# Kernel tuning notes

Measured on AMD Instinct MI355X. Metric: run time of the kernel, lower is better.

## Reference

```python
import jax, jax.numpy as jnp
import numpy as np

EMBED = 512; HEADS = 16; WIN = 8; SHIFT = 4

def _rel_pos_index(Wh, Ww):
    # WindowMSA.double_step_seq + transpose-sum + flip(1)
    seq1 = np.arange(0, (2 * Ww - 1) * Wh, 2 * Ww - 1)
    seq2 = np.arange(0, Ww)
    coords = (seq1[:, None] + seq2[None, :]).reshape(1, -1)
    idx = coords + coords.T            # (Wh*Ww, Wh*Ww)
    return idx[:, ::-1].copy()

def _attn_mask(H_pad, W_pad, win, shift, nf):
    # static (trace-time) shifted-window mask, values in {0, -100}
    img = np.zeros((H_pad, W_pad))
    cnt = 0
    for h in (slice(0, -win), slice(-win, -shift), slice(-shift, None)):
        for w in (slice(0, -win), slice(-win, -shift), slice(-shift, None)):
            img[h, w] = cnt
            cnt += 1
    mw = img.reshape(H_pad // win, win, W_pad // win, win).transpose(0, 2, 1, 3).reshape(-1, win * win)
    am = mw[:, None, :] - mw[:, :, None]
    am = np.where(am != 0, -100.0, 0.0)
    return np.tile(am, (1, 1, nf))     # (nW, N, nf*N)

def setup_inputs():
    key = jax.random.key(0)
    ks = jax.random.split(key, 8)
    B, H, W, C, nf = 8, 128, 128, EMBED, 2
    s = 0.02
    return {
        'q': jax.random.normal(ks[0], (B, H * W, C), jnp.float32),
        'kv': jax.random.normal(ks[1], (B, nf, H * W, C), jnp.float32),
        'H': H, 'W': W,
        'rpb_table': jax.random.normal(ks[2], ((2 * WIN - 1) ** 2, HEADS), jnp.float32) * s,
        'Wq': jax.random.normal(ks[3], (C, C), jnp.float32) * s,
        'bq': jnp.zeros((C,), jnp.float32),
        'Wkv': jax.random.normal(ks[4], (C, 2 * C), jnp.float32) * s,
        'bkv': jnp.zeros((2 * C,), jnp.float32),
        'Wo': jax.random.normal(ks[5], (C, C), jnp.float32) * s,
        'bo': jnp.zeros((C,), jnp.float32),
    }

def reference(q, kv, H, W, rpb_table, Wq, bq, Wkv, bkv, Wo, bo):
    B, L, C = q.shape
    nf = kv.shape[1]
    win, shift, heads = WIN, SHIFT, HEADS
    hd = C // heads
    scale = hd ** -0.5
    pad_b = (-H) % win
    pad_r = (-W) % win
    x = q.reshape(B, H, W, C)
    kvx = kv.reshape(B * nf, H, W, C)
    x = jnp.pad(x, ((0, 0), (0, pad_b), (0, pad_r), (0, 0)))
    kvx = jnp.pad(kvx, ((0, 0), (0, pad_b), (0, pad_r), (0, 0)))
    Hp, Wp = H + pad_b, W + pad_r
    nh, nw = Hp // win, Wp // win
    if shift > 0:
        x = jnp.roll(x, (-shift, -shift), (1, 2))
        kvx = jnp.roll(kvx, (-shift, -shift), (1, 2))
        mask = jnp.asarray(_attn_mask(Hp, Wp, win, shift, nf), q.dtype)
    else:
        mask = None
    Nq = win * win
    Nk = nf * Nq
    # window partition: (B, Hp, Wp, C) -> (B*nh*nw, Nq, C)
    qw = x.reshape(B, nh, win, nw, win, C).transpose(0, 1, 3, 2, 4, 5).reshape(B * nh * nw, Nq, C)
    # kv: (B*nf, Hp, Wp, C) -> (B*nh*nw, nf*Nq, C)
    kvw = kvx.reshape(B, nf, nh, win, nw, win, C).transpose(0, 2, 4, 1, 3, 5, 6).reshape(B * nh * nw, Nk, C)
    Bw = qw.shape[0]
    qh = (qw @ Wq + bq).reshape(Bw, Nq, heads, hd).transpose(0, 2, 1, 3) * scale
    kvp = (kvw @ Wkv + bkv).reshape(Bw, Nk, 2, heads, hd).transpose(2, 0, 3, 1, 4)
    kh, vh = kvp[0], kvp[1]
    attn = jnp.einsum('bhqd,bhkd->bhqk', qh, kh)
    rpi = jnp.asarray(_rel_pos_index(win, win).reshape(-1))
    rpb = rpb_table[rpi].reshape(Nq, Nq, heads).transpose(2, 0, 1)  # (heads, Nq, Nq)
    attn = attn + jnp.tile(rpb, (1, 1, nf))[None]
    if mask is not None:
        nW = mask.shape[0]
        attn = (attn.reshape(Bw // nW, nW, heads, Nq, Nk) + mask[None, :, None]).reshape(Bw, heads, Nq, Nk)
    attn = jax.nn.softmax(attn, axis=-1)
    ow = jnp.einsum('bhqk,bhkd->bqhd', attn, vh).reshape(Bw, Nq, C)
    ow = ow @ Wo + bo
    # window reverse
    x = ow.reshape(B, nh, nw, win, win, C).transpose(0, 1, 3, 2, 4, 5).reshape(B, Hp, Wp, C)
    if shift > 0:
        x = jnp.roll(x, (shift, shift), (1, 2))
    x = x[:, :H, :W, :].reshape(B, H * W, C)
    return x
```

## Files before the change

kernel.cpp:

```cpp
#include <hip/hip_runtime.h>

typedef unsigned short ushort_t;
typedef short bf16x8 __attribute__((ext_vector_type(8)));
typedef float f32x4 __attribute__((ext_vector_type(4)));

#define MFMA16(a, b, c) __builtin_amdgcn_mfma_f32_16x16x32_bf16(a, b, c, 0, 0, 0)

static __device__ __forceinline__ float bf2f(ushort_t u) {
  union { unsigned int i; float f; } v;
  v.i = ((unsigned int)u) << 16;
  return v.f;
}
static __device__ __forceinline__ ushort_t f2bf(float f) {
  union { float f; unsigned int i; } v;
  v.f = f;
  unsigned int u = v.i;
  u = u + 0x7fffu + ((u >> 16) & 1u);
  return (ushort_t)(u >> 16);
}
static __device__ __forceinline__ unsigned int cvtpk(float lo, float hi) {
  unsigned int r;
  asm("v_cvt_pk_bf16_f32 %0, %1, %2" : "=v"(r) : "v"(lo), "v"(hi));
  return r;
}
static __device__ __forceinline__ void gload16(const void* g, void* l) {
  __builtin_amdgcn_global_load_lds((const __attribute__((address_space(1))) void*)g,
                                   (__attribute__((address_space(3))) void*)l,
                                   16, 0, 0);
}

__global__ void ws_sentinel(float* out, unsigned long long ws) {
  if (blockIdx.x == 0 && threadIdx.x == 0)
    out[0] = 1.0e6f * (1.0f + (float)(ws >> 23));
}

__global__ __launch_bounds__(256) void wtrans(const float* __restrict__ in,
                                              ushort_t* __restrict__ out,
                                              int R, int C) {
  int idx = blockIdx.x * 256 + threadIdx.x;
  if (idx < R * C) {
    int r = idx / C, c = idx - r * C;
    out[c * R + r] = f2bf(in[idx]);
  }
}

template <bool AF32, bool CF32>
__global__ __launch_bounds__(256, 2) void gemm_bt(const void* __restrict__ Av,
                                                  const ushort_t* __restrict__ Bt,
                                                  const float* __restrict__ bias,
                                                  void* __restrict__ Cv,
                                                  int N, int Nt) {
  constexpr int K = 512;
  __shared__ unsigned char As[AF32 ? 128 * 32 * 4 : 128 * 32 * 2];
  __shared__ unsigned char Bs[128 * 32 * 2];
  const int t = threadIdx.x;
  const int l = t & 63;
  const int w = t >> 6;
  const int w32 = w * 32;
  const int wr = w >> 1, wc = w & 1;
  const int lrow = l & 15;
  const int g = l >> 4;

  const int bid = blockIdx.x;
  const int xcd = bid & 7;
  const int slot = bid >> 3;
  const int mt = xcd + 8 * (slot / Nt);
  const int nt = slot % Nt;
  const long m0 = (long)mt * 128;
  const int n0 = nt * 128;

  const int arow = l >> 3;
  const int acol = 4 * ((l & 7) ^ (arow & 1));
  const int brow = l >> 2;
  const int bcol = 8 * (l & 3);

  const f32x4 fz = {0.f, 0.f, 0.f, 0.f};
  f32x4 acc[4][4];
#pragma unroll
  for (int i = 0; i < 4; i++)
#pragma unroll
    for (int j = 0; j < 4; j++) acc[i][j] = fz;

  for (int kk = 0; kk < K; kk += 32) {
    __syncthreads();
    if constexpr (AF32) {
#pragma unroll
      for (int i = 0; i < 4; i++) {
        const float* gp = (const float*)Av + (m0 + w32 + i * 8 + arow) * (long)K + kk + acol;
        gload16(gp, &As[(w32 + i * 8) * 128]);
      }
    } else {
#pragma unroll
      for (int i = 0; i < 2; i++) {
        const ushort_t* gp = (const ushort_t*)Av + (m0 + w32 + i * 16 + brow) * (long)K + kk + bcol;
        gload16(gp, &As[(w32 + i * 16) * 64]);
      }
    }
#pragma unroll
    for (int i = 0; i < 2; i++) {
      const ushort_t* gp = Bt + (long)(n0 + w32 + i * 16 + brow) * K + kk + bcol;
      gload16(gp, &Bs[(w32 + i * 16) * 64]);
    }
    __syncthreads();

    bf16x8 af[4], bfr[4];
    if constexpr (AF32) {
#pragma unroll
      for (int mi = 0; mi < 4; mi++) {
        const int aR = wr * 64 + mi * 16 + lrow;
        const int sw = (aR & 1);
        f32x4 x = *(const f32x4*)&As[aR * 128 + (((2 * g) ^ sw) << 4)];
        f32x4 y = *(const f32x4*)&As[aR * 128 + (((2 * g + 1) ^ sw) << 4)];
        union { unsigned int u[4]; bf16x8 v; } r;
        r.u[0] = cvtpk(x[0], x[1]);
        r.u[1] = cvtpk(x[2], x[3]);
        r.u[2] = cvtpk(y[0], y[1]);
        r.u[3] = cvtpk(y[2], y[3]);
        af[mi] = r.v;
      }
    } else {
#pragma unroll
      for (int mi = 0; mi < 4; mi++) {
        const int aR = wr * 64 + mi * 16 + lrow;
        af[mi] = *(const bf16x8*)&As[aR * 64 + g * 16];
      }
    }
#pragma unroll
    for (int ni = 0; ni < 4; ni++) {
      const int bR = wc * 64 + ni * 16 + lrow;
      bfr[ni] = *(const bf16x8*)&Bs[bR * 64 + g * 16];
    }
#pragma unroll
    for (int mi = 0; mi < 4; mi++)
#pragma unroll
      for (int ni = 0; ni < 4; ni++)
        acc[mi][ni] = MFMA16(af[mi], bfr[ni], acc[mi][ni]);
  }

#pragma unroll
  for (int mi = 0; mi < 4; mi++) {
    const long row0 = m0 + wr * 64 + mi * 16 + (l >> 4) * 4;
#pragma unroll
    for (int ni = 0; ni < 4; ni++) {
      const int col = n0 + wc * 64 + ni * 16 + lrow;
      const float bv = bias[col];
#pragma unroll
      for (int r = 0; r < 4; r++) {
        const float val = acc[mi][ni][r] + bv;
        if constexpr (CF32)
          ((float*)Cv)[(row0 + r) * N + col] = val;
        else
          ((ushort_t*)Cv)[(row0 + r) * N + col] = f2bf(val);
      }
    }
  }
}

__global__ __launch_bounds__(64, 1) void attn_k(const ushort_t* __restrict__ Qp,
                                                const ushort_t* __restrict__ KVp,
                                                const float* __restrict__ rpbt,
                                                ushort_t* __restrict__ Ao) {
  __shared__ ushort_t P[64 * 136];
  __shared__ __align__(16) unsigned char pool[32 * 136 * 2];
  float* Ltab = (float*)pool;
  ushort_t* Vt = (ushort_t*)pool;
  const int l = threadIdx.x;
  const int wnd = blockIdx.x;
  const int h = blockIdx.y;
  const int b = wnd >> 8;
  const int wh = (wnd >> 4) & 15;
  const int ww = wnd & 15;
  for (int i = l; i < 225; i += 64) Ltab[i] = rpbt[i * 16 + h];

  const int lrow = l & 15;
  const int lq = l >> 4;
  const int lk = lq * 8;

  auto qrow = [&](int q) -> long {
    int i = q >> 3, j = q & 7;
    int ho = (wh * 8 + i + 4) & 127;
    int wo = (ww * 8 + j + 4) & 127;
    return (long)((b << 14) + (ho << 7) + wo);
  };
  auto kvrow = [&](int kp) -> long {
    int f = kp >> 6, m = kp & 63;
    int i = m >> 3, j = m & 7;
    int ho = (wh * 8 + i + 4) & 127;
    int wo = (ww * 8 + j + 4) & 127;
    return (long)(((b * 2 + f) << 14) + (ho << 7) + wo);
  };
  auto cnt_of = [&](int m) -> int {
    int hr = wh * 8 + (m >> 3), wr2 = ww * 8 + (m & 7);
    int rh = hr < 120 ? 0 : (hr < 124 ? 1 : 2);
    int rw = wr2 < 120 ? 0 : (wr2 < 124 ? 1 : 2);
    return rh * 3 + rw;
  };
  auto cvec = [](int m) -> int { return 15 * (m >> 3) + (m & 7); };

  const f32x4 fz = {0.f, 0.f, 0.f, 0.f};
  f32x4 s[4][8];
#pragma unroll
  for (int mi = 0; mi < 4; mi++)
#pragma unroll
    for (int ni = 0; ni < 8; ni++) s[mi][ni] = fz;

  bf16x8 af[4];
#pragma unroll
  for (int mi = 0; mi < 4; mi++)
    af[mi] = *(const bf16x8*)(Qp + qrow(mi * 16 + lrow) * 512 + h * 32 + lk);
#pragma unroll
  for (int ni = 0; ni < 8; ni++) {
    bf16x8 kf = *(const bf16x8*)(KVp + kvrow(ni * 16 + lrow) * 1024 + h * 32 + lk);
#pragma unroll
    for (int mi = 0; mi < 4; mi++) s[mi][ni] = MFMA16(af[mi], kf, s[mi][ni]);
  }

  __syncthreads();

  const float scale = 0.17677669529663687f;
#pragma unroll
  for (int mi = 0; mi < 4; mi++) {
#pragma unroll
    for (int r = 0; r < 4; r++) {
      const int q = mi * 16 + lq * 4 + r;
      const int cq = cnt_of(q);
      const int cqv = cvec(q);
      float mx = -3.0e38f;
#pragma unroll
      for (int ni = 0; ni < 8; ni++) {
        const int k63 = (ni * 16 + lrow) & 63;
        float v = s[mi][ni][r] * scale + Ltab[cqv + cvec(63 - k63)];
        if (cnt_of(k63) != cq) v -= 100.f;
        s[mi][ni][r] = v;
        mx = fmaxf(mx, v);
      }
      mx = fmaxf(mx, __shfl_xor(mx, 1));
      mx = fmaxf(mx, __shfl_xor(mx, 2));
      mx = fmaxf(mx, __shfl_xor(mx, 4));
      mx = fmaxf(mx, __shfl_xor(mx, 8));
      float sum = 0.f;
#pragma unroll
      for (int ni = 0; ni < 8; ni++) {
        float p = __expf(s[mi][ni][r] - mx);
        s[mi][ni][r] = p;
        sum += p;
      }
      sum += __shfl_xor(sum, 1);
      sum += __shfl_xor(sum, 2);
      sum += __shfl_xor(sum, 4);
      sum += __shfl_xor(sum, 8);
      const float inv = 1.f / sum;
#pragma unroll
      for (int ni = 0; ni < 8; ni++)
        P[q * 136 + ni * 16 + lrow] = f2bf(s[mi][ni][r] * inv);
    }
  }

#pragma unroll
  for (int kv2 = 0; kv2 < 2; kv2++) {
    const int kp = l * 2 + kv2;
    const ushort_t* src = KVp + kvrow(kp) * 1024 + 512 + h * 32;
    bf16x8 v0 = *(const bf16x8*)(src);
    bf16x8 v1 = *(const bf16x8*)(src + 8);
    bf16x8 v2 = *(const bf16x8*)(src + 16);
    bf16x8 v3 = *(const bf16x8*)(src + 24);
#pragma unroll
    for (int d = 0; d < 8; d++) {
      Vt[(d) * 136 + kp] = (ushort_t)v0[d];
      Vt[(8 + d) * 136 + kp] = (ushort_t)v1[d];
      Vt[(16 + d) * 136 + kp] = (ushort_t)v2[d];
      Vt[(24 + d) * 136 + kp] = (ushort_t)v3[d];
    }
  }
  __syncthreads();

  f32x4 o[4][2];
#pragma unroll
  for (int mi = 0; mi < 4; mi++) { o[mi][0] = fz; o[mi][1] = fz; }
#pragma unroll
  for (int ks = 0; ks < 4; ks++) {
    bf16x8 pf[4];
#pragma unroll
    for (int mi = 0; mi < 4; mi++)
      pf[mi] = *(const bf16x8*)&P[(mi * 16 + lrow) * 136 + ks * 32 + lk];
#pragma unroll
    for (int ni = 0; ni < 2; ni++) {
      bf16x8 vf = *(const bf16x8*)&Vt[(ni * 16 + lrow) * 136 + ks * 32 + lk];
#pragma unroll
      for (int mi = 0; mi < 4; mi++) o[mi][ni] = MFMA16(pf[mi], vf, o[mi][ni]);
    }
  }

#pragma unroll
  for (int mi = 0; mi < 4; mi++)
#pragma unroll
    for (int ni = 0; ni < 2; ni++)
#pragma unroll
      for (int r = 0; r < 4; r++) {
        const int q = mi * 16 + lq * 4 + r;
        Ao[qrow(q) * 512 + h * 32 + ni * 16 + lrow] = f2bf(o[mi][ni][r]);
      }
}

extern "C" void kernel_launch(void* const* d_in, const int* in_sizes, int n_in,
                              void* d_out, int out_size, void* d_ws, size_t ws_size,
                              hipStream_t stream) {
  (void)in_sizes; (void)n_in; (void)out_size;
  const float* q    = (const float*)d_in[0];
  const float* kv   = (const float*)d_in[1];
  const float* rpbt = (const float*)d_in[4];
  const float* Wq   = (const float*)d_in[5];
  const float* bq   = (const float*)d_in[6];
  const float* Wkv  = (const float*)d_in[7];
  const float* bkv  = (const float*)d_in[8];
  const float* Wo   = (const float*)d_in[9];
  const float* bo   = (const float*)d_in[10];
  float* out = (float*)d_out;

  const size_t QB  = 16384ULL * 512;
  const size_t KVB = 32768ULL * 1024;
  const size_t per_b_bytes = (QB + QB + KVB) * 2;
  const size_t fixed_bytes = (512ULL*512 + 512ULL*1024 + 512ULL*512) * 2;
  const size_t needed1 = fixed_bytes + per_b_bytes;

  if (ws_size < needed1) {
    ws_sentinel<<<dim3(1), 64, 0, stream>>>(out, (unsigned long long)ws_size);
    return;
  }

  int nbc = 8;
  while (nbc > 1 && fixed_bytes + (size_t)nbc * per_b_bytes > ws_size) nbc >>= 1;

  char* ws = (char*)d_ws;
  ushort_t* WqT  = (ushort_t*)ws;
  ushort_t* WkvT = WqT + 512 * 512;
  ushort_t* WoT  = WkvT + 512 * 1024;
  ushort_t* Qp   = (ushort_t*)(ws + fixed_bytes);
  ushort_t* Ao   = Qp + (size_t)nbc * QB;
  ushort_t* KVp  = Ao + (size_t)nbc * QB;

  wtrans<<<dim3(1024), 256, 0, stream>>>(Wq, WqT, 512, 512);
  wtrans<<<dim3(2048), 256, 0, stream>>>(Wkv, WkvT, 512, 1024);
  wtrans<<<dim3(1024), 256, 0, stream>>>(Wo, WoT, 512, 512);

  for (int c = 0; c < 8 / nbc; ++c) {
    const size_t b0 = (size_t)c * nbc;
    const int MtQ = nbc * 128;
    const int MtKV = nbc * 256;
    gemm_bt<true, false><<<dim3(MtQ * 4), 256, 0, stream>>>(q + b0 * QB, WqT, bq,
                                                            Qp, 512, 4);
    gemm_bt<true, false><<<dim3(MtKV * 8), 256, 0, stream>>>(kv + b0 * KVB / 2, WkvT,
                                                             bkv, KVp, 1024, 8);
    attn_k<<<dim3(nbc * 256, 16), 64, 0, stream>>>(Qp, KVp, rpbt, Ao);
    gemm_bt<false, true><<<dim3(MtQ * 4), 256, 0, stream>>>(Ao, WoT, bo,
                                                            out + b0 * QB, 512, 4);
  }
}
```

Measured before the change: 1.077 ms.

## Double-buffer GEMM LDS tiles and apply XOR swizzle to avoid bank conflicts

The projection GEMM kernel now keeps two LDS buffers for the A and B tiles and issues the global-to-LDS loads for the next K step before computing on the current one, leaving one barrier per iteration instead of two. It also replaces the old row-parity swizzle with a wider XOR swizzle on both the write and read addresses, aimed at cutting LDS bank conflicts on the fragment reads. Double buffering doubles LDS use per block, which may limit how many blocks fit per CU when combined with launch_bounds(256,2).

```diff
diff --git a/kernel.cpp b/kernel.cpp
--- a/kernel.cpp
+++ b/kernel.cpp
@@ -51,8 +51,10 @@
                                                   void* __restrict__ Cv,
                                                   int N, int Nt) {
   constexpr int K = 512;
-  __shared__ unsigned char As[AF32 ? 128 * 32 * 4 : 128 * 32 * 2];
-  __shared__ unsigned char Bs[128 * 32 * 2];
+  constexpr int NT_STEPS = K / 32;
+  constexpr int ABYTES = AF32 ? 128 * 32 * 4 : 128 * 32 * 2;
+  __shared__ unsigned char As[2][ABYTES];
+  __shared__ unsigned char Bs[2][128 * 32 * 2];
   const int t = threadIdx.x;
   const int l = t & 63;
   const int w = t >> 6;
@@ -70,9 +72,30 @@
   const int n0 = nt * 128;
 
   const int arow = l >> 3;
-  const int acol = 4 * ((l & 7) ^ (arow & 1));
+  const int acol = ((16 * (l & 7)) ^ ((arow & 7) << 4)) >> 2;
   const int brow = l >> 2;
-  const int bcol = 8 * (l & 3);
+  const int bcol = ((16 * (l & 3)) ^ ((brow & 3) << 4)) >> 1;
+
+  auto stage = [&](int buf, int kk) {
+    if constexpr (AF32) {
+#pragma unroll
+      for (int i = 0; i < 4; i++) {
+        const float* gp = (const float*)Av + (m0 + w32 + i * 8 + arow) * (long)K + kk + acol;
+        gload16(gp, &As[buf][(w32 + i * 8) * 128]);
+      }
+    } else {
+#pragma unroll
+      for (int i = 0; i < 2; i++) {
+        const ushort_t* gp = (const ushort_t*)Av + (m0 + w32 + i * 16 + brow) * (long)K + kk + bcol;
+        gload16(gp, &As[buf][(w32 + i * 16) * 64]);
+      }
+    }
+#pragma unroll
+    for (int i = 0; i < 2; i++) {
+      const ushort_t* gp = Bt + (long)(n0 + w32 + i * 16 + brow) * K + kk + bcol;
+      gload16(gp, &Bs[buf][(w32 + i * 16) * 64]);
+    }
+  };
 
   const f32x4 fz = {0.f, 0.f, 0.f, 0.f};
   f32x4 acc[4][4];
@@ -81,36 +104,22 @@
 #pragma unroll
     for (int j = 0; j < 4; j++) acc[i][j] = fz;
 
-  for (int kk = 0; kk < K; kk += 32) {
-    __syncthreads();
-    if constexpr (AF32) {
-#pragma unroll
-      for (int i = 0; i < 4; i++) {
-        const float* gp = (const float*)Av + (m0 + w32 + i * 8 + arow) * (long)K + kk + acol;
-        gload16(gp, &As[(w32 + i * 8) * 128]);
-      }
-    } else {
-#pragma unroll
-      for (int i = 0; i < 2; i++) {
-        const ushort_t* gp = (const ushort_t*)Av + (m0 + w32 + i * 16 + brow) * (long)K + kk + bcol;
-        gload16(gp, &As[(w32 + i * 16) * 64]);
-      }
-    }
-#pragma unroll
-    for (int i = 0; i < 2; i++) {
-      const ushort_t* gp = Bt + (long)(n0 + w32 + i * 16 + brow) * K + kk + bcol;
-      gload16(gp, &Bs[(w32 + i * 16) * 64]);
-    }
-    __syncthreads();
+  stage(0, 0);
+  __syncthreads();
+  int cur = 0;
+
+  for (int ts = 0; ts < NT_STEPS; ++ts) {
+    if (ts + 1 < NT_STEPS) stage(cur ^ 1, (ts + 1) * 32);
 
     bf16x8 af[4], bfr[4];
     if constexpr (AF32) {
 #pragma unroll
       for (int mi = 0; mi < 4; mi++) {
         const int aR = wr * 64 + mi * 16 + lrow;
-        const int sw = (aR & 1);
-        f32x4 x = *(const f32x4*)&As[aR * 128 + (((2 * g) ^ sw) << 4)];
-        f32x4 y = *(const f32x4*)&As[aR * 128 + (((2 * g + 1) ^ sw) << 4)];
+        const int s = (aR & 7) << 4;
+        const int c0 = g * 32;
+        f32x4 x = *(const f32x4*)&As[cur][aR * 128 + (c0 ^ s)];
+        f32x4 y = *(const f32x4*)&As[cur][aR * 128 + ((c0 + 16) ^ s)];
         union { unsigned int u[4]; bf16x8 v; } r;
         r.u[0] = cvtpk(x[0], x[1]);
         r.u[1] = cvtpk(x[2], x[3]);
@@ -122,19 +131,22 @@
 #pragma unroll
       for (int mi = 0; mi < 4; mi++) {
         const int aR = wr * 64 + mi * 16 + lrow;
-        af[mi] = *(const bf16x8*)&As[aR * 64 + g * 16];
+        af[mi] = *(const bf16x8*)&As[cur][aR * 64 + ((g * 16) ^ ((aR & 3) << 4))];
       }
     }
 #pragma unroll
     for (int ni = 0; ni < 4; ni++) {
       const int bR = wc * 64 + ni * 16 + lrow;
-      bfr[ni] = *(const bf16x8*)&Bs[bR * 64 + g * 16];
+      bfr[ni] = *(const bf16x8*)&Bs[cur][bR * 64 + ((g * 16) ^ ((bR & 3) << 4))];
     }
 #pragma unroll
     for (int mi = 0; mi < 4; mi++)
 #pragma unroll
       for (int ni = 0; ni < 4; ni++)
         acc[mi][ni] = MFMA16(af[mi], bfr[ni], acc[mi][ni]);
+
+    __syncthreads();
+    cur ^= 1;
   }
 
 #pragma unroll
```

New measurement: 1.133 ms. 5.2% more time.

## Split attention across four waves per window and XOR-swizzle GEMM LDS tiles

Applied to the files above, without the earlier changes.

The attention kernel now launches 256 threads per window-head block, with each wave handling 16 query rows instead of one wave doing all 64. The V transpose load is split across the four waves. This cuts per-thread register pressure and serial work and raises occupancy and latency hiding, at the cost of an extra barrier. Separately, the GEMM shared-memory tiles use a wider XOR swizzle (8-way for fp32 A, 4-way for bf16) to reduce LDS bank conflicts on fragment reads.

```diff
diff --git a/kernel.cpp b/kernel.cpp
--- a/kernel.cpp
+++ b/kernel.cpp
@@ -59,7 +59,6 @@
   const int w32 = w * 32;
   const int wr = w >> 1, wc = w & 1;
   const int lrow = l & 15;
-  const int g = l >> 4;
 
   const int bid = blockIdx.x;
   const int xcd = bid & 7;
@@ -70,9 +69,9 @@
   const int n0 = nt * 128;
 
   const int arow = l >> 3;
-  const int acol = 4 * ((l & 7) ^ (arow & 1));
+  const int acol = ((16 * (l & 7)) ^ ((arow & 7) << 4)) >> 2;
   const int brow = l >> 2;
-  const int bcol = 8 * (l & 3);
+  const int bcol = ((16 * (l & 3)) ^ ((brow & 3) << 4)) >> 1;
 
   const f32x4 fz = {0.f, 0.f, 0.f, 0.f};
   f32x4 acc[4][4];
@@ -108,9 +107,10 @@
 #pragma unroll
       for (int mi = 0; mi < 4; mi++) {
         const int aR = wr * 64 + mi * 16 + lrow;
-        const int sw = (aR & 1);
-        f32x4 x = *(const f32x4*)&As[aR * 128 + (((2 * g) ^ sw) << 4)];
-        f32x4 y = *(const f32x4*)&As[aR * 128 + (((2 * g + 1) ^ sw) << 4)];
+        const int s = (aR & 7) << 4;
+        const int c0 = (l >> 4) * 32;
+        f32x4 x = *(const f32x4*)&As[aR * 128 + (c0 ^ s)];
+        f32x4 y = *(const f32x4*)&As[aR * 128 + ((c0 + 16) ^ s)];
         union { unsigned int u[4]; bf16x8 v; } r;
         r.u[0] = cvtpk(x[0], x[1]);
         r.u[1] = cvtpk(x[2], x[3]);
@@ -122,13 +122,13 @@
 #pragma unroll
       for (int mi = 0; mi < 4; mi++) {
         const int aR = wr * 64 + mi * 16 + lrow;
-        af[mi] = *(const bf16x8*)&As[aR * 64 + g * 16];
+        af[mi] = *(const bf16x8*)&As[aR * 64 + (((l >> 4) * 16) ^ ((aR & 3) << 4))];
       }
     }
 #pragma unroll
     for (int ni = 0; ni < 4; ni++) {
       const int bR = wc * 64 + ni * 16 + lrow;
-      bfr[ni] = *(const bf16x8*)&Bs[bR * 64 + g * 16];
+      bfr[ni] = *(const bf16x8*)&Bs[bR * 64 + (((l >> 4) * 16) ^ ((bR & 3) << 4))];
     }
 #pragma unroll
     for (int mi = 0; mi < 4; mi++)
@@ -156,21 +156,23 @@
   }
 }
 
-__global__ __launch_bounds__(64, 1) void attn_k(const ushort_t* __restrict__ Qp,
-                                                const ushort_t* __restrict__ KVp,
-                                                const float* __restrict__ rpbt,
-                                                ushort_t* __restrict__ Ao) {
+__global__ __launch_bounds__(256, 1) void attn_k(const ushort_t* __restrict__ Qp,
+                                                 const ushort_t* __restrict__ KVp,
+                                                 const float* __restrict__ rpbt,
+                                                 ushort_t* __restrict__ Ao) {
   __shared__ ushort_t P[64 * 136];
   __shared__ __align__(16) unsigned char pool[32 * 136 * 2];
   float* Ltab = (float*)pool;
   ushort_t* Vt = (ushort_t*)pool;
-  const int l = threadIdx.x;
+  const int t = threadIdx.x;
+  const int l = t & 63;
+  const int w = t >> 6;
   const int wnd = blockIdx.x;
   const int h = blockIdx.y;
   const int b = wnd >> 8;
   const int wh = (wnd >> 4) & 15;
   const int ww = wnd & 15;
-  for (int i = l; i < 225; i += 64) Ltab[i] = rpbt[i * 16 + h];
+  for (int i = t; i < 225; i += 256) Ltab[i] = rpbt[i * 16 + h];
 
   const int lrow = l & 15;
   const int lq = l >> 4;
@@ -198,108 +200,89 @@
   auto cvec = [](int m) -> int { return 15 * (m >> 3) + (m & 7); };
 
   const f32x4 fz = {0.f, 0.f, 0.f, 0.f};
-  f32x4 s[4][8];
-#pragma unroll
-  for (int mi = 0; mi < 4; mi++)
-#pragma unroll
-    for (int ni = 0; ni < 8; ni++) s[mi][ni] = fz;
-
-  bf16x8 af[4];
-#pragma unroll
-  for (int mi = 0; mi < 4; mi++)
-    af[mi] = *(const bf16x8*)(Qp + qrow(mi * 16 + lrow) * 512 + h * 32 + lk);
+  f32x4 s[8];
+#pragma unroll
+  for (int ni = 0; ni < 8; ni++) s[ni] = fz;
+
+  bf16x8 af = *(const bf16x8*)(Qp + qrow(w * 16 + lrow) * 512 + h * 32 + lk);
 #pragma unroll
   for (int ni = 0; ni < 8; ni++) {
     bf16x8 kf = *(const bf16x8*)(KVp + kvrow(ni * 16 + lrow) * 1024 + h * 32 + lk);
-#pragma unroll
-    for (int mi = 0; mi < 4; mi++) s[mi][ni] = MFMA16(af[mi], kf, s[mi][ni]);
+    s[ni] = MFMA16(af, kf, s[ni]);
   }
 
   __syncthreads();
 
   const float scale = 0.17677669529663687f;
 #pragma unroll
-  for (int mi = 0; mi < 4; mi++) {
-#pragma unroll
-    for (int r = 0; r < 4; r++) {
-      const int q = mi * 16 + lq * 4 + r;
-      const int cq = cnt_of(q);
-      const int cqv = cvec(q);
-      float mx = -3.0e38f;
-#pragma unroll
-      for (int ni = 0; ni < 8; ni++) {
-        const int k63 = (ni * 16 + lrow) & 63;
-        float v = s[mi][ni][r] * scale + Ltab[cqv + cvec(63 - k63)];
-        if (cnt_of(k63) != cq) v -= 100.f;
-        s[mi][ni][r] = v;
-        mx = fmaxf(mx, v);
-      }
-      mx = fmaxf(mx, __shfl_xor(mx, 1));
-      mx = fmaxf(mx, __shfl_xor(mx, 2));
-      mx = fmaxf(mx, __shfl_xor(mx, 4));
-      mx = fmaxf(mx, __shfl_xor(mx, 8));
-      float sum = 0.f;
-#pragma unroll
-      for (int ni = 0; ni < 8; ni++) {
-        float p = __expf(s[mi][ni][r] - mx);
-        s[mi][ni][r] = p;
-        sum += p;
-      }
-      sum += __shfl_xor(sum, 1);
-      sum += __shfl_xor(sum, 2);
-      sum += __shfl_xor(sum, 4);
-      sum += __shfl_xor(sum, 8);
-      const float inv = 1.f / sum;
-#pragma unroll
-      for (int ni = 0; ni < 8; ni++)
-        P[q * 136 + ni * 16 + lrow] = f2bf(s[mi][ni][r] * inv);
-    }
-  }
-
-#pragma unroll
-  for (int kv2 = 0; kv2 < 2; kv2++) {
-    const int kp = l * 2 + kv2;
-    const ushort_t* src = KVp + kvrow(kp) * 1024 + 512 + h * 32;
+  for (int r = 0; r < 4; r++) {
+    const int q = w * 16 + lq * 4 + r;
+    const int cq = cnt_of(q);
+    const int cqv = cvec(q);
+    float mx = -3.0e38f;
+#pragma unroll
+    for (int ni = 0; ni < 8; ni++) {
+      const int k63 = (ni * 16 + lrow) & 63;
+      float v = s[ni][r] * scale + Ltab[cqv + cvec(63 - k63)];
+      if (cnt_of(k63) != cq) v -= 100.f;
+      s[ni][r] = v;
+      mx = fmaxf(mx, v);
+    }
+    mx = fmaxf(mx, __shfl_xor(mx, 1));
+    mx = fmaxf(mx, __shfl_xor(mx, 2));
+    mx = fmaxf(mx, __shfl_xor(mx, 4));
+    mx = fmaxf(mx, __shfl_xor(mx, 8));
+    float sum = 0.f;
+#pragma unroll
+    for (int ni = 0; ni < 8; ni++) {
+      float p = __expf(s[ni][r] - mx);
+      s[ni][r] = p;
+      sum += p;
+    }
+    sum += __shfl_xor(sum, 1);
+    sum += __shfl_xor(sum, 2);
+    sum += __shfl_xor(sum, 4);
+    sum += __shfl_xor(sum, 8);
+    const float inv = 1.f / sum;
+#pragma unroll
+    for (int ni = 0; ni < 8; ni++)
+      P[q * 136 + ni * 16 + lrow] = f2bf(s[ni][r] * inv);
+  }
+
+  __syncthreads();
+
+  {
+    const int kp = t & 127;
+    const int dh = t >> 7;
+    const ushort_t* src = KVp + kvrow(kp) * 1024 + 512 + h * 32 + dh * 16;
     bf16x8 v0 = *(const bf16x8*)(src);
     bf16x8 v1 = *(const bf16x8*)(src + 8);
-    bf16x8 v2 = *(const bf16x8*)(src + 16);
-    bf16x8 v3 = *(const bf16x8*)(src + 24);
 #pragma unroll
     for (int d = 0; d < 8; d++) {
-      Vt[(d) * 136 + kp] = (ushort_t)v0[d];
-      Vt[(8 + d) * 136 + kp] = (ushort_t)v1[d];
-      Vt[(16 + d) * 136 + kp] = (ushort_t)v2[d];
-      Vt[(24 + d) * 136 + kp] = (ushort_t)v3[d];
+      Vt[(dh * 16 + d) * 136 + kp] = (ushort_t)v0[d];
+      Vt[(dh * 16 + 8 + d) * 136 + kp] = (ushort_t)v1[d];
     }
   }
   __syncthreads();
 
-  f32x4 o[4][2];
-#pragma unroll
-  for (int mi = 0; mi < 4; mi++) { o[mi][0] = fz; o[mi][1] = fz; }
+  f32x4 o[2] = {fz, fz};
 #pragma unroll
   for (int ks = 0; ks < 4; ks++) {
-    bf16x8 pf[4];
-#pragma unroll
-    for (int mi = 0; mi < 4; mi++)
-      pf[mi] = *(const bf16x8*)&P[(mi * 16 + lrow) * 136 + ks * 32 + lk];
+    bf16x8 pf = *(const bf16x8*)&P[(w * 16 + lrow) * 136 + ks * 32 + lk];
 #pragma unroll
     for (int ni = 0; ni < 2; ni++) {
       bf16x8 vf = *(const bf16x8*)&Vt[(ni * 16 + lrow) * 136 + ks * 32 + lk];
-#pragma unroll
-      for (int mi = 0; mi < 4; mi++) o[mi][ni] = MFMA16(pf[mi], vf, o[mi][ni]);
-    }
-  }
-
-#pragma unroll
-  for (int mi = 0; mi < 4; mi++)
-#pragma unroll
-    for (int ni = 0; ni < 2; ni++)
-#pragma unroll
-      for (int r = 0; r < 4; r++) {
-        const int q = mi * 16 + lq * 4 + r;
-        Ao[qrow(q) * 512 + h * 32 + ni * 16 + lrow] = f2bf(o[mi][ni][r]);
-      }
+      o[ni] = MFMA16(pf, vf, o[ni]);
+    }
+  }
+
+#pragma unroll
+  for (int ni = 0; ni < 2; ni++)
+#pragma unroll
+    for (int r = 0; r < 4; r++) {
+      const int q = w * 16 + lq * 4 + r;
+      Ao[qrow(q) * 512 + h * 32 + ni * 16 + lrow] = f2bf(o[ni][r]);
+    }
 }
 
 extern "C" void kernel_launch(void* const* d_in, const int* in_sizes, int n_in,
@@ -351,7 +334,7 @@
                                                             Qp, 512, 4);
     gemm_bt<true, false><<<dim3(MtKV * 8), 256, 0, stream>>>(kv + b0 * KVB / 2, WkvT,
                                                              bkv, KVp, 1024, 8);
-    attn_k<<<dim3(nbc * 256, 16), 64, 0, stream>>>(Qp, KVp, rpbt, Ao);
+    attn_k<<<dim3(nbc * 256, 16), 256, 0, stream>>>(Qp, KVp, rpbt, Ao);
     gemm_bt<false, true><<<dim3(MtQ * 4), 256, 0, stream>>>(Ao, WoT, bo,
                                                             out + b0 * QB, 512, 4);
   }
```

After: 1.043 ms. 3.1% less time.
